# Kernel optimization log

Hardware: AMD Instinct MI355X
Metric: run time of the kernel (lower is better)

The kernel has to match this reference:

```python
import jax, jax.numpy as jnp
import numpy as np

WINDOW = 16  # hardcoded in module __init__

B, S, E, H = 2, 2048, 1024, 16
HD = E // H


def setup_inputs() -> dict:
    key = jax.random.key(0)
    k1, k2, k3, k4, k5, k6 = jax.random.split(key, 6)
    input_embeddings = jax.random.normal(k1, (B, S, E), dtype=jnp.float32)
    token_ids = jax.random.randint(k2, (B, S), 0, 32000, dtype=jnp.int64)
    # nn.MultiheadAttention parameters: packed in_proj (3E, E) + bias, out_proj (E, E) + bias
    in_proj_weight = jax.random.normal(k3, (3 * E, E), dtype=jnp.float32) * 0.02
    in_proj_bias = jax.random.normal(k4, (3 * E,), dtype=jnp.float32) * 0.02
    out_proj_weight = jax.random.normal(k5, (E, E), dtype=jnp.float32) * 0.02
    out_proj_bias = jax.random.normal(k6, (E,), dtype=jnp.float32) * 0.02
    return {
        "input_embeddings": input_embeddings,
        "token_ids": token_ids,
        "in_proj_weight": in_proj_weight,
        "in_proj_bias": in_proj_bias,
        "out_proj_weight": out_proj_weight,
        "out_proj_bias": out_proj_bias,
    }


def _blocked_mask(seq_len: int) -> jnp.ndarray:
    # Module sets mask[i, j] = True for j in [i - WINDOW, i] (17 positions).
    # PyTorch bool attn_mask: True = NOT allowed to attend.
    i = jnp.arange(seq_len)[:, None]
    j = jnp.arange(seq_len)[None, :]
    return (j <= i) & (j >= i - WINDOW)  # [S, S] bool, True = masked out


def reference(input_embeddings, token_ids, in_proj_weight, in_proj_bias,
              out_proj_weight, out_proj_bias):
    x = input_embeddings  # [B, S, E]
    b, s, e = x.shape
    # Packed QKV projection (torch Linear: y = x W^T + b)
    qkv = jnp.einsum('bse,fe->bsf', x, in_proj_weight) + in_proj_bias  # [B, S, 3E]
    q, k, v = jnp.split(qkv, 3, axis=-1)
    # Split heads: [B, H, S, HD]
    q = q.reshape(b, s, H, HD).transpose(0, 2, 1, 3)
    k = k.reshape(b, s, H, HD).transpose(0, 2, 1, 3)
    v = v.reshape(b, s, H, HD).transpose(0, 2, 1, 3)
    scale = 1.0 / jnp.sqrt(jnp.asarray(HD, dtype=x.dtype))
    scores = jnp.einsum('bhqd,bhkd->bhqk', q * scale, k)  # [B, H, S, S]
    blocked = _blocked_mask(s)  # True = masked
    scores = jnp.where(blocked[None, None, :, :], -jnp.inf, scores)
    attn = jax.nn.softmax(scores, axis=-1)
    ctx = jnp.einsum('bhqk,bhkd->bhqd', attn, v)  # [B, H, S, HD]
    ctx = ctx.transpose(0, 2, 1, 3).reshape(b, s, e)
    out = jnp.einsum('bse,fe->bsf', ctx, out_proj_weight) + out_proj_bias
    return out
```

## Files before the change

### kernel.cpp

```cpp
#include <hip/hip_runtime.h>

typedef __attribute__((ext_vector_type(8))) __bf16 bf16x8;
typedef __attribute__((ext_vector_type(4))) float f32x4;
typedef __attribute__((ext_vector_type(16))) float f32x16;
typedef unsigned short u16;
typedef unsigned int u32;

#define MFMA16(a, b, c) __builtin_amdgcn_mfma_f32_16x16x32_bf16((a), (b), (c), 0, 0, 0)
#define MFMA32(a, b, c) __builtin_amdgcn_mfma_f32_32x32x16_bf16((a), (b), (c), 0, 0, 0)

__device__ __forceinline__ u16 f2bf(float f) {
  return (u16)((__float_as_uint(f) + 0x8000u) >> 16);
}

#define BDIM 2
#define SDIM 2048
#define EDIM 1024
#define HDIM 16
#define HD 64
#define MDIM (BDIM * SDIM)

#define SC_C1 0.1803368801111355f

typedef __attribute__((address_space(3))) void lds_void;
typedef __attribute__((address_space(1))) void g_void;

__device__ __forceinline__ void async_lds16(const void* g, void* lds_byte) {
  __builtin_amdgcn_global_load_lds((const g_void*)g, (lds_void*)lds_byte, 16, 0, 0);
}

__global__ __launch_bounds__(256) void cvt3_kernel(
    const float* __restrict__ s0, u16* __restrict__ d0, int n0,
    const float* __restrict__ s1, u16* __restrict__ d1, int n1,
    const float* __restrict__ s2, u16* __restrict__ d2, int n2) {
  int i = (blockIdx.x * 256 + threadIdx.x) * 8;
  const float* s;
  u16* d;
  if (i < n0) {
    s = s0 + i; d = d0 + i;
  } else if (i < n0 + n1) {
    s = s1 + (i - n0); d = d1 + (i - n0);
  } else if (i < n0 + n1 + n2) {
    s = s2 + (i - n0 - n1); d = d2 + (i - n0 - n1);
  } else {
    return;
  }
  float4 f0 = *(const float4*)(s);
  float4 f1 = *(const float4*)(s + 4);
  union { uint4 u; u16 h[8]; } o;
  o.h[0] = f2bf(f0.x); o.h[1] = f2bf(f0.y); o.h[2] = f2bf(f0.z); o.h[3] = f2bf(f0.w);
  o.h[4] = f2bf(f1.x); o.h[5] = f2bf(f1.y); o.h[6] = f2bf(f1.z); o.h[7] = f2bf(f1.w);
  *(uint4*)(d) = o.u;
}

__global__ __launch_bounds__(256) void gemm_qkv_kernel(
    const u16* __restrict__ X, const u16* __restrict__ W,
    const float* __restrict__ bias, u16* __restrict__ qb,
    u16* __restrict__ kb, u16* __restrict__ vtb) {
  __shared__ __align__(16) u16 As[128 * 64];
  __shared__ __align__(16) u16 Bs[128 * 64];
  const int m0 = blockIdx.x * 128, n0 = blockIdx.y * 128;
  const bool isV = (n0 >= 2 * EDIM);
  const int t = threadIdx.x;
  const int l = t & 63;
  const int quad = l >> 4, col = l & 15;
  const int wid = t >> 6;
  const int mh = wid & 1, nh = wid >> 1;
  const int wofs = (t & 192) << 4;
  f32x4 acc[4][4] = {};
  const u16* Ab = X + (size_t)m0 * EDIM;
  const u16* Bb = W + (size_t)n0 * EDIM;
  char* AsB = (char*)As;
  char* BsB = (char*)Bs;

  for (int k0 = 0; k0 < EDIM; k0 += 64) {
    __syncthreads();
#pragma unroll
    for (int p = 0; p < 4; p++) {
      int idx = p * 256 + t;
      int row = idx >> 3;
      int gch = (idx & 7) ^ (row & 7);
      async_lds16(Ab + (size_t)row * EDIM + k0 + gch * 8, AsB + p * 4096 + wofs);
      async_lds16(Bb + (size_t)row * EDIM + k0 + gch * 8, BsB + p * 4096 + wofs);
    }
    __syncthreads();
#pragma unroll
    for (int kk = 0; kk < 2; kk++) {
      bf16x8 af[4], bfr[4];
#pragma unroll
      for (int i = 0; i < 4; i++) {
        int ra = 64 * mh + 16 * i + col;
        af[i] = *(const bf16x8*)&As[ra * 64 + (((kk * 4 + quad) ^ (ra & 7)) * 8)];
        int rb = 64 * nh + 16 * i + col;
        bfr[i] = *(const bf16x8*)&Bs[rb * 64 + (((kk * 4 + quad) ^ (rb & 7)) * 8)];
      }
      if (isV) {
#pragma unroll
        for (int i = 0; i < 4; i++)
#pragma unroll
          for (int j = 0; j < 4; j++)
            acc[i][j] = MFMA16(bfr[i], af[j], acc[i][j]);
      } else {
#pragma unroll
        for (int i = 0; i < 4; i++)
#pragma unroll
          for (int j = 0; j < 4; j++)
            acc[i][j] = MFMA16(af[i], bfr[j], acc[i][j]);
      }
    }
  }

  if (isV) {
#pragma unroll
    for (int i = 0; i < 4; i++)
#pragma unroll
      for (int j = 0; j < 4; j++)
#pragma unroll
        for (int r = 0; r < 4; r++) {
          int n = n0 + 64 * nh + 16 * i + quad * 4 + r;
          int m = m0 + 64 * mh + 16 * j + col;
          float val = acc[i][j][r] + bias[n];
          int e = n & 1023;
          int hh = e >> 6, d = e & 63;
          int bb = m >> 11, s = m & 2047;
          vtb[(((size_t)(bb * HDIM + hh)) * HD + d) * SDIM + s] = f2bf(val);
        }
  } else {
    const float qscale = (n0 < EDIM) ? SC_C1 : 1.0f;
#pragma unroll
    for (int i = 0; i < 4; i++)
#pragma unroll
      for (int j = 0; j < 4; j++)
#pragma unroll
        for (int r = 0; r < 4; r++) {
          int m = m0 + 64 * mh + 16 * i + quad * 4 + r;
          int n = n0 + 64 * nh + 16 * j + col;
          float val = (acc[i][j][r] + bias[n]) * qscale;
          int which = n >> 10, e = n & 1023;
          int hh = e >> 6, d = e & 63;
          int bb = m >> 11, s = m & 2047;
          u16* dst = (which == 0) ? qb : kb;
          dst[(((size_t)(bb * HDIM + hh)) * SDIM + s) * HD + d] = f2bf(val);
        }
  }
}

__global__ __launch_bounds__(256) void attn_kernel(
    const u16* __restrict__ qg, const u16* __restrict__ kg,
    const u16* __restrict__ vtg, u16* __restrict__ ctx) {
  __shared__ __align__(16) u16 KB[2][64 * 64];
  __shared__ __align__(16) u16 VB[3][64 * 64];

  const int bh = blockIdx.x;
  const int q0 = blockIdx.y * 128;
  const int t = threadIdx.x;
  const int wid = t >> 6, l = t & 63;
  const int col = l & 31, half = l >> 5;
  const size_t base = (size_t)bh * SDIM * HD;

  const int qw0 = q0 + 32 * wid;
  const int qi = qw0 + col;

  bf16x8 bq[4];
  {
    const u16* qp = qg + base + (size_t)qi * HD + half * 8;
#pragma unroll
    for (int f = 0; f < 4; f++) bq[f] = *(const bf16x8*)(qp + f * 16);
  }
  asm volatile("" : "+v"(bq[0]), "+v"(bq[1]), "+v"(bq[2]), "+v"(bq[3]));

  const int srow = t >> 3;
  const int g = (t & 7) ^ (srow & 7);
  const u16* kptr = kg + base + (size_t)srow * HD + g * 8;
  const u16* vptr = vtg + base + (size_t)srow * SDIM + g * 8;
  const int wofs = (t & 192) << 4;

  auto stageK = [&](int kt, int buf) {
    char* d = (char*)KB[buf] + wofs;
    async_lds16(kptr + (size_t)(kt * 64) * HD, d);
    async_lds16(kptr + (size_t)(kt * 64 + 32) * HD, d + 4096);
  };
  auto stageV = [&](int kt, int buf) {
    char* d = (char*)VB[buf] + wofs;
    async_lds16(vptr + kt * 64, d);
    async_lds16(vptr + (size_t)32 * SDIM + kt * 64, d + 4096);
  };

  auto qkt = [&](const u16* Kt, f32x16 (&sco)[2]) {
#pragma unroll
    for (int s = 0; s < 2; s++)
#pragma unroll
      for (int f = 0; f < 4; f++) {
        int kr = 32 * s + col;
        int phys = (2 * f + half) ^ (kr & 7);
        bf16x8 kf = *(const bf16x8*)&Kt[kr * 64 + phys * 8];
        sco[s] = MFMA32(kf, bq[f], sco[s]);
      }
  };

  float ps0 = 0.f, ps1 = 0.f, ps2 = 0.f, ps3 = 0.f;
  f32x16 oacc[2] = {};

  auto smax = [&](int kt, f32x16 (&cur)[2], bool band, u32 (&w)[2][8]) {
#pragma unroll
    for (int s = 0; s < 2; s++) {
      float p[16];
#pragma unroll
      for (int r = 0; r < 16; r++) {
        float v = cur[s][r];
        if (band) {
          int j = kt * 64 + 32 * s + (r & 3) + 8 * (r >> 2) + 4 * half;
          if (j <= qi && j + 16 >= qi) v = -1.0e30f;
        }
        p[r] = __builtin_exp2f(v);
      }
#pragma unroll
      for (int r = 0; r < 16; r++) {
        if ((r & 3) == 0) ps0 += p[r];
        else if ((r & 3) == 1) ps1 += p[r];
        else if ((r & 3) == 2) ps2 += p[r];
        else ps3 += p[r];
      }
#pragma unroll
      for (int j = 0; j < 8; j++) {
        u32 wv;
        asm("v_cvt_pk_bf16_f32 %0, %1, %2" : "=v"(wv) : "v"(p[2 * j]), "v"(p[2 * j + 1]));
        w[s][j] = wv;
      }
    }
  };

  auto pv = [&](const u16* Vt, u32 (&w)[2][8]) {
#pragma unroll
    for (int s = 0; s < 2; s++)
#pragma unroll
      for (int b2 = 0; b2 < 2; b2++) {
        u32 x0 = w[s][4 * b2 + 0], x1 = w[s][4 * b2 + 1];
        u32 y0 = w[s][4 * b2 + 2], y1 = w[s][4 * b2 + 3];
        asm("v_permlane32_swap_b32 %0, %1" : "+v"(x0), "+v"(y0));
        asm("v_permlane32_swap_b32 %0, %1" : "+v"(x1), "+v"(y1));
        uint4 pw;
        pw.x = x0; pw.y = x1; pw.z = y0; pw.w = y1;
        bf16x8 pa = __builtin_bit_cast(bf16x8, pw);
        int ks = 2 * s + b2;
#pragma unroll
        for (int dt = 0; dt < 2; dt++) {
          int vr = 32 * dt + col;
          int phys = (2 * ks + half) ^ (vr & 7);
          bf16x8 vf = *(const bf16x8*)&Vt[vr * 64 + phys * 8];
          oacc[dt] = MFMA32(vf, pa, oacc[dt]);
        }
      }
  };

  const int NT = SDIM / 64;

  auto body = [&](int kt, f32x16 (&cur)[2], f32x16 (&nxt)[2]) {
    __syncthreads();
    if (kt + 1 < NT) {
      nxt[0] = (f32x16){};
      nxt[1] = (f32x16){};
      qkt(KB[(kt + 1) & 1], nxt);
    }
    if (kt + 2 < NT) {
      stageK(kt + 2, kt & 1);
      stageV(kt + 2, (unsigned)(kt + 2) % 3u);
    }
    u32 w[2][8];
    bool band = (kt * 64 <= qw0 + 31) && (kt * 64 + 63 >= qw0 - 16);
    smax(kt, cur, band, w);
    pv(VB[(unsigned)kt % 3u], w);
  };

  f32x16 scA[2] = {}, scB[2] = {};
  stageK(0, 0);
  stageV(0, 0);
  __syncthreads();
  qkt(KB[0], scA);
  stageK(1, 1);
  stageV(1, 1);

#pragma unroll 1
  for (int kt = 0; kt < NT; kt += 2) {
    body(kt, scA, scB);
    body(kt + 1, scB, scA);
  }

  float psum = (ps0 + ps1) + (ps2 + ps3);
  psum += __shfl_xor(psum, 32, 64);
  float linv = 1.0f / psum;

  const int b = bh >> 4, h = bh & 15;
  u16* cbase = ctx + ((size_t)(b * SDIM + qi)) * EDIM + h * HD;
#pragma unroll
  for (int dt = 0; dt < 2; dt++)
#pragma unroll
    for (int a = 0; a < 4; a++) {
      float v0 = oacc[dt][4 * a + 0] * linv, v1 = oacc[dt][4 * a + 1] * linv;
      float v2 = oacc[dt][4 * a + 2] * linv, v3 = oacc[dt][4 * a + 3] * linv;
      u32 w0, w1;
      asm("v_cvt_pk_bf16_f32 %0, %1, %2" : "=v"(w0) : "v"(v0), "v"(v1));
      asm("v_cvt_pk_bf16_f32 %0, %1, %2" : "=v"(w1) : "v"(v2), "v"(v3));
      uint2 st;
      st.x = w0; st.y = w1;
      *(uint2*)(cbase + 32 * dt + 8 * a + 4 * half) = st;
    }
}

__global__ __launch_bounds__(256) void gemm_out_kernel(
    const u16* __restrict__ A, const u16* __restrict__ W,
    const float* __restrict__ bias, float* __restrict__ out) {
  __shared__ __align__(16) u16 As[128 * 64];
  __shared__ __align__(16) u16 Bs[128 * 64];
  const int m0 = blockIdx.x * 128, n0 = blockIdx.y * 128;
  const int t = threadIdx.x;
  const int l = t & 63;
  const int quad = l >> 4, col = l & 15;
  const int wid = t >> 6;
  const int mh = wid & 1, nh = wid >> 1;
  const int wofs = (t & 192) << 4;
  f32x4 acc[4][4] = {};
  const u16* Ab = A + (size_t)m0 * EDIM;
  const u16* Bb = W + (size_t)n0 * EDIM;
  char* AsB = (char*)As;
  char* BsB = (char*)Bs;

  for (int k0 = 0; k0 < EDIM; k0 += 64) {
    __syncthreads();
#pragma unroll
    for (int p = 0; p < 4; p++) {
      int idx = p * 256 + t;
      int row = idx >> 3;
      int gch = (idx & 7) ^ (row & 7);
      async_lds16(Ab + (size_t)row * EDIM + k0 + gch * 8, AsB + p * 4096 + wofs);
      async_lds16(Bb + (size_t)row * EDIM + k0 + gch * 8, BsB + p * 4096 + wofs);
    }
    __syncthreads();
#pragma unroll
    for (int kk = 0; kk < 2; kk++) {
      bf16x8 af[4], bfr[4];
#pragma unroll
      for (int i = 0; i < 4; i++) {
        int ra = 64 * mh + 16 * i + col;
        af[i] = *(const bf16x8*)&As[ra * 64 + (((kk * 4 + quad) ^ (ra & 7)) * 8)];
        int rb = 64 * nh + 16 * i + col;
        bfr[i] = *(const bf16x8*)&Bs[rb * 64 + (((kk * 4 + quad) ^ (rb & 7)) * 8)];
      }
#pragma unroll
      for (int i = 0; i < 4; i++)
#pragma unroll
        for (int j = 0; j < 4; j++)
          acc[i][j] = MFMA16(af[i], bfr[j], acc[i][j]);
    }
  }

#pragma unroll
  for (int i = 0; i < 4; i++)
#pragma unroll
    for (int j = 0; j < 4; j++)
#pragma unroll
      for (int r = 0; r < 4; r++) {
        int m = m0 + 64 * mh + 16 * i + quad * 4 + r;
        int n = n0 + 64 * nh + 16 * j + col;
        out[(size_t)m * EDIM + n] = acc[i][j][r] + bias[n];
      }
}

extern "C" void kernel_launch(void* const* d_in, const int* in_sizes, int n_in,
                              void* d_out, int out_size, void* d_ws,
                              size_t ws_size, hipStream_t stream) {
  const float* x = (const float*)d_in[0];
  const float* in_w = (const float*)d_in[2];
  const float* in_b = (const float*)d_in[3];
  const float* out_w = (const float*)d_in[4];
  const float* out_b = (const float*)d_in[5];
  float* out = (float*)d_out;

  char* ws = (char*)d_ws;
  u16* Xb  = (u16*)ws;
  u16* ctx = (u16*)ws;
  u16* qb  = (u16*)(ws + (size_t)( 8 << 20));
  u16* kb  = (u16*)(ws + (size_t)(16 << 20));
  u16* vtb = (u16*)(ws + (size_t)(24 << 20));
  u16* Wib = (u16*)(ws + (size_t)(32 << 20));
  u16* Wob = (u16*)(ws + (size_t)(38 << 20));

  const int nX = MDIM * EDIM;
  const int nWi = 3 * EDIM * EDIM;
  const int nWo = EDIM * EDIM;
  cvt3_kernel<<<(nX + nWi + nWo) / 8 / 256, 256, 0, stream>>>(
      x, Xb, nX, in_w, Wib, nWi, out_w, Wob, nWo);

  gemm_qkv_kernel<<<dim3(MDIM / 128, 3 * EDIM / 128), 256, 0, stream>>>(
      Xb, Wib, in_b, qb, kb, vtb);
  attn_kernel<<<dim3(BDIM * HDIM, SDIM / 128), 256, 0, stream>>>(qb, kb, vtb, ctx);
  gemm_out_kernel<<<dim3(MDIM / 128, EDIM / 128), 256, 0, stream>>>(
      ctx, Wob, out_b, out);
}
```

Before: 219.7 us.

## Unroll attention loop by four with precomputed LDS offsets, setprio, smaller out-GEMM tile

The attention kernel gets a fourth V buffer so the main loop can be unrolled by four with compile-time buffer indices, removing the modulo-3 indexing. LDS fragment offsets are precomputed once, MFMA sections are wrapped in s_setprio, score accumulators are zeroed through the first MFMA instead of explicit clears, and the raw hardware exp2 builtin replaces the generic one. Separately, the output GEMM tile is halved in N (128x64) so twice as many blocks are launched, trading per-block data reuse for better occupancy and fill across CUs. The extra V buffer adds LDS use per block.

Measured after the change: 232.0 us. 5.6% more time.

```diff
diff --git a/kernel.cpp b/kernel.cpp
--- a/kernel.cpp
+++ b/kernel.cpp
@@ -149,7 +149,7 @@
     const u16* __restrict__ qg, const u16* __restrict__ kg,
     const u16* __restrict__ vtg, u16* __restrict__ ctx) {
   __shared__ __align__(16) u16 KB[2][64 * 64];
-  __shared__ __align__(16) u16 VB[3][64 * 64];
+  __shared__ __align__(16) u16 VB[4][64 * 64];
 
   const int bh = blockIdx.x;
   const int q0 = blockIdx.y * 128;
@@ -186,16 +186,28 @@
     async_lds16(vptr + (size_t)32 * SDIM + kt * 64, d + 4096);
   };
 
-  auto qkt = [&](const u16* Kt, f32x16 (&sco)[2]) {
-#pragma unroll
-    for (int s = 0; s < 2; s++)
+  const int c7 = col & 7;
+  int off[4];
+#pragma unroll
+  for (int x = 0; x < 4; x++)
+    off[x] = col * 128 + ((((x << 1) | half) ^ c7) << 4);
+
+  const char* KB0 = (const char*)&KB[0][0];
+  const char* VB0 = (const char*)&VB[0][0];
+
+  const f32x16 Z = {};
+
+  auto qkt = [&](int kbuf, f32x16 (&sco)[2]) {
+    __builtin_amdgcn_s_setprio(1);
+#pragma unroll
+    for (int s = 0; s < 2; s++) {
 #pragma unroll
       for (int f = 0; f < 4; f++) {
-        int kr = 32 * s + col;
-        int phys = (2 * f + half) ^ (kr & 7);
-        bf16x8 kf = *(const bf16x8*)&Kt[kr * 64 + phys * 8];
-        sco[s] = MFMA32(kf, bq[f], sco[s]);
-      }
+        bf16x8 kf = *(const bf16x8*)(KB0 + kbuf * 8192 + s * 4096 + off[f]);
+        sco[s] = (f == 0) ? MFMA32(kf, bq[0], Z) : MFMA32(kf, bq[f], sco[s]);
+      }
+    }
+    __builtin_amdgcn_s_setprio(0);
   };
 
   float ps0 = 0.f, ps1 = 0.f, ps2 = 0.f, ps3 = 0.f;
@@ -212,7 +224,7 @@
           int j = kt * 64 + 32 * s + (r & 3) + 8 * (r >> 2) + 4 * half;
           if (j <= qi && j + 16 >= qi) v = -1.0e30f;
         }
-        p[r] = __builtin_exp2f(v);
+        p[r] = __builtin_amdgcn_exp2f(v);
       }
 #pragma unroll
       for (int r = 0; r < 16; r++) {
@@ -230,7 +242,7 @@
     }
   };
 
-  auto pv = [&](const u16* Vt, u32 (&w)[2][8]) {
+  auto pv = [&](int vbuf, u32 (&w)[2][8]) {
 #pragma unroll
     for (int s = 0; s < 2; s++)
 #pragma unroll
@@ -243,47 +255,46 @@
         pw.x = x0; pw.y = x1; pw.z = y0; pw.w = y1;
         bf16x8 pa = __builtin_bit_cast(bf16x8, pw);
         int ks = 2 * s + b2;
+        __builtin_amdgcn_s_setprio(1);
 #pragma unroll
         for (int dt = 0; dt < 2; dt++) {
-          int vr = 32 * dt + col;
-          int phys = (2 * ks + half) ^ (vr & 7);
-          bf16x8 vf = *(const bf16x8*)&Vt[vr * 64 + phys * 8];
+          bf16x8 vf = *(const bf16x8*)(VB0 + vbuf * 8192 + dt * 4096 + off[ks]);
           oacc[dt] = MFMA32(vf, pa, oacc[dt]);
         }
+        __builtin_amdgcn_s_setprio(0);
       }
   };
 
   const int NT = SDIM / 64;
 
-  auto body = [&](int kt, f32x16 (&cur)[2], f32x16 (&nxt)[2]) {
+  auto body = [&](int kt, int kbufN, int vbufC, int vbufS, f32x16 (&cur)[2],
+                  f32x16 (&nxt)[2]) {
     __syncthreads();
-    if (kt + 1 < NT) {
-      nxt[0] = (f32x16){};
-      nxt[1] = (f32x16){};
-      qkt(KB[(kt + 1) & 1], nxt);
-    }
+    if (kt + 1 < NT) qkt(kbufN, nxt);
     if (kt + 2 < NT) {
-      stageK(kt + 2, kt & 1);
-      stageV(kt + 2, (unsigned)(kt + 2) % 3u);
+      stageK(kt + 2, kbufN ^ 1);
+      stageV(kt + 2, vbufS);
     }
     u32 w[2][8];
     bool band = (kt * 64 <= qw0 + 31) && (kt * 64 + 63 >= qw0 - 16);
     smax(kt, cur, band, w);
-    pv(VB[(unsigned)kt % 3u], w);
-  };
-
-  f32x16 scA[2] = {}, scB[2] = {};
+    pv(vbufC, w);
+  };
+
+  f32x16 scA[2], scB[2];
   stageK(0, 0);
   stageV(0, 0);
   __syncthreads();
-  qkt(KB[0], scA);
+  qkt(0, scA);
   stageK(1, 1);
   stageV(1, 1);
 
 #pragma unroll 1
-  for (int kt = 0; kt < NT; kt += 2) {
-    body(kt, scA, scB);
-    body(kt + 1, scB, scA);
+  for (int kt4 = 0; kt4 < NT; kt4 += 4) {
+    body(kt4 + 0, 1, 0, 2, scA, scB);
+    body(kt4 + 1, 0, 1, 3, scB, scA);
+    body(kt4 + 2, 1, 2, 0, scA, scB);
+    body(kt4 + 3, 0, 3, 1, scB, scA);
   }
 
   float psum = (ps0 + ps1) + (ps2 + ps3);
@@ -311,15 +322,15 @@
     const u16* __restrict__ A, const u16* __restrict__ W,
     const float* __restrict__ bias, float* __restrict__ out) {
   __shared__ __align__(16) u16 As[128 * 64];
-  __shared__ __align__(16) u16 Bs[128 * 64];
-  const int m0 = blockIdx.x * 128, n0 = blockIdx.y * 128;
+  __shared__ __align__(16) u16 Bs[64 * 64];
+  const int m0 = blockIdx.x * 128, n0 = blockIdx.y * 64;
   const int t = threadIdx.x;
   const int l = t & 63;
   const int quad = l >> 4, col = l & 15;
   const int wid = t >> 6;
   const int mh = wid & 1, nh = wid >> 1;
   const int wofs = (t & 192) << 4;
-  f32x4 acc[4][4] = {};
+  f32x4 acc[4][2] = {};
   const u16* Ab = A + (size_t)m0 * EDIM;
   const u16* Bb = W + (size_t)n0 * EDIM;
   char* AsB = (char*)As;
@@ -333,23 +344,32 @@
       int row = idx >> 3;
       int gch = (idx & 7) ^ (row & 7);
       async_lds16(Ab + (size_t)row * EDIM + k0 + gch * 8, AsB + p * 4096 + wofs);
+    }
+#pragma unroll
+    for (int p = 0; p < 2; p++) {
+      int idx = p * 256 + t;
+      int row = idx >> 3;
+      int gch = (idx & 7) ^ (row & 7);
       async_lds16(Bb + (size_t)row * EDIM + k0 + gch * 8, BsB + p * 4096 + wofs);
     }
     __syncthreads();
 #pragma unroll
     for (int kk = 0; kk < 2; kk++) {
-      bf16x8 af[4], bfr[4];
+      bf16x8 af[4], bfr[2];
 #pragma unroll
       for (int i = 0; i < 4; i++) {
         int ra = 64 * mh + 16 * i + col;
         af[i] = *(const bf16x8*)&As[ra * 64 + (((kk * 4 + quad) ^ (ra & 7)) * 8)];
-        int rb = 64 * nh + 16 * i + col;
-        bfr[i] = *(const bf16x8*)&Bs[rb * 64 + (((kk * 4 + quad) ^ (rb & 7)) * 8)];
+      }
+#pragma unroll
+      for (int j = 0; j < 2; j++) {
+        int rb = 32 * nh + 16 * j + col;
+        bfr[j] = *(const bf16x8*)&Bs[rb * 64 + (((kk * 4 + quad) ^ (rb & 7)) * 8)];
       }
 #pragma unroll
       for (int i = 0; i < 4; i++)
 #pragma unroll
-        for (int j = 0; j < 4; j++)
+        for (int j = 0; j < 2; j++)
           acc[i][j] = MFMA16(af[i], bfr[j], acc[i][j]);
     }
   }
@@ -357,11 +377,11 @@
 #pragma unroll
   for (int i = 0; i < 4; i++)
 #pragma unroll
-    for (int j = 0; j < 4; j++)
+    for (int j = 0; j < 2; j++)
 #pragma unroll
       for (int r = 0; r < 4; r++) {
         int m = m0 + 64 * mh + 16 * i + quad * 4 + r;
-        int n = n0 + 64 * nh + 16 * j + col;
+        int n = n0 + 32 * nh + 16 * j + col;
         out[(size_t)m * EDIM + n] = acc[i][j][r] + bias[n];
       }
 }
@@ -394,6 +414,6 @@
   gemm_qkv_kernel<<<dim3(MDIM / 128, 3 * EDIM / 128), 256, 0, stream>>>(
       Xb, Wib, in_b, qb, kb, vtb);
   attn_kernel<<<dim3(BDIM * HDIM, SDIM / 128), 256, 0, stream>>>(qb, kb, vtb, ctx);
-  gemm_out_kernel<<<dim3(MDIM / 128, EDIM / 128), 256, 0, stream>>>(
+  gemm_out_kernel<<<dim3(MDIM / 128, EDIM / 64), 256, 0, stream>>>(
       ctx, Wob, out_b, out);
 }
```
